# Optimization experiments

Hardware: AMD Instinct MI355X
Metric: run time of the kernel (lower is better)

Reference implementation:

```python
import jax, jax.numpy as jnp
import numpy as np

CUTOFF = 5.0

def cubic_cutoff(d):
    # f(0)=1, f(y)=0, smooth first derivatives at both ends
    y = CUTOFF
    xc = 1.0 - 1.5 * (d * d) / (y * y) + 0.5 * (d * d * d) / (y * y * y)
    return jnp.where(d <= 0.0, 1.0, jnp.where(d >= y, 0.0, xc))


def setup_inputs() -> dict:
    key = jax.random.key(0)
    ks = jax.random.split(key, 16)
    B, N, H = 64, 64, 128
    h = jax.random.normal(ks[0], (B, N, H), jnp.float32)
    x = jax.random.uniform(ks[1], (B, N, 3), jnp.float32) * 10.0  # 10A box -> partial neighbor sparsity
    node_mask = jnp.ones((B, N), dtype=bool)
    h0 = jax.random.normal(ks[2], (B, N, H), jnp.float32)
    s = lambda fin: 1.0 / np.sqrt(fin)
    # edge_mlp: Linear(2H+1 -> H), SiLU, Linear(H -> H), SiLU
    We1 = jax.random.normal(ks[3], (2 * H + 1, H), jnp.float32) * s(2 * H + 1)
    be1 = jnp.zeros((H,), jnp.float32)
    We2 = jax.random.normal(ks[4], (H, H), jnp.float32) * s(H)
    be2 = jnp.zeros((H,), jnp.float32)
    # node_mlp: Linear(H + residual_nf + H = 3H -> H), SiLU, Linear(H -> H)
    Wn1 = jax.random.normal(ks[5], (3 * H, H), jnp.float32) * s(3 * H)
    bn1 = jnp.zeros((H,), jnp.float32)
    Wn2 = jax.random.normal(ks[6], (H, H), jnp.float32) * s(H)
    bn2 = jnp.zeros((H,), jnp.float32)
    # coord_mlp: Linear(H -> H), SiLU, Linear(H -> 1, no bias, xavier gain=0.001)
    Wc1 = jax.random.normal(ks[7], (H, H), jnp.float32) * s(H)
    bc1 = jnp.zeros((H,), jnp.float32)
    Wc2 = jax.random.normal(ks[8], (H, 1), jnp.float32) * (0.001 * s(H))
    return {"h": h, "x": x, "node_mask": node_mask, "h0": h0,
            "We1": We1, "be1": be1, "We2": We2, "be2": be2,
            "Wn1": Wn1, "bn1": bn1, "Wn2": Wn2, "bn2": bn2,
            "Wc1": Wc1, "bc1": bc1, "Wc2": Wc2}


def reference(h, x, node_mask, h0, We1, be1, We2, be2, Wn1, bn1, Wn2, bn2, Wc1, bc1, Wc2):
    B, N, H = h.shape
    # pairwise distances; distances are detached in the torch default path
    diff = x[:, :, None, :] - x[:, None, :, :]                     # [B,N,N,3]
    d = jax.lax.stop_gradient(jnp.sqrt(jnp.sum(diff * diff, -1)))  # [B,N,N]
    eye = jnp.eye(N, dtype=bool)[None]
    mask = (node_mask[:, :, None] & node_mask[:, None, :]
            & (d < CUTOFF) & (~eye))                               # [B,N,N]
    maskf = mask.astype(h.dtype)
    # edge model: feat[b,j,k] = [h[b,j], h[b,k], d^2]
    feat = jnp.concatenate([
        jnp.broadcast_to(h[:, :, None, :], (B, N, N, H)),
        jnp.broadcast_to(h[:, None, :, :], (B, N, N, H)),
        (d * d)[..., None]], axis=-1)                              # [B,N,N,2H+1]
    e = jax.nn.silu(feat @ We1 + be1)
    e = jax.nn.silu(e @ We2 + be2)
    mij = e * (cubic_cutoff(d) * maskf)[..., None]                 # [B,N,N,H]
    # node model: sum messages into receiver j
    mi = jnp.sum(mij, axis=2)                                      # [B,N,H]
    nfeat = jnp.concatenate([h, mi, h0], axis=-1)                  # [B,N,3H]
    h_out = jax.nn.silu(nfeat @ Wn1 + bn1) @ Wn2 + bn2
    h_new = h + h_out                                              # recurrent
    # coord model (scatter-add semantics of the intended math)
    phi = jax.nn.silu(mij @ Wc1 + bc1) @ Wc2                       # [B,N,N,1]
    C = 1.0 / (N - 1.0)
    x_up = C * jnp.sum(diff * phi * maskf[..., None], axis=2)      # [B,N,3]
    x_new = jnp.clip(x + x_up, -1000.0, 1000.0)
    return (h_new, x_new)
```

## Files before the change

kernel.cpp:

```cpp
#include <hip/hip_runtime.h>

#define Hh 128
#define Nn 64

typedef _Float16 f16x8 __attribute__((ext_vector_type(8)));
typedef float f32x4 __attribute__((ext_vector_type(4)));

__device__ __forceinline__ float silu_f(float v){
    return v * __builtin_amdgcn_rcpf(1.0f + __expf(-v));
}
__device__ __forceinline__ int swz(int row, int cb){ return row*256 + (cb ^ ((row & 7) << 4)); }

#define WT_BYTES (9*32768)

__global__ __launch_bounds__(128) void k_w(
    const float* __restrict__ We1, const float* __restrict__ We2, const float* __restrict__ Wc1,
    const float* __restrict__ Wn1, const float* __restrict__ Wn2, char* __restrict__ wT)
{
    if (blockIdx.x == 128){
        if (threadIdx.x < 16){
            f16x8 v;
            #pragma unroll
            for (int i=0;i<8;i++) v[i] = (_Float16)We1[256*Hh + threadIdx.x*8 + i];
            *(f16x8*)(wT + 8*32768 + threadIdx.x*16) = v;
        }
        return;
    }
    const int id  = blockIdx.x*128 + threadIdx.x;
    const int mat = id >> 11;
    const int r   = id & 2047;
    const int n   = r >> 4;
    const int kg  = r & 15;
    const float* __restrict__ src;
    int koff = 0;
    switch (mat){
        case 0: src = We2; break;
        case 1: src = Wc1; break;
        case 2: src = Wn1; break;
        case 3: src = Wn1; koff = 128; break;
        case 4: src = Wn1; koff = 256; break;
        case 5: src = Wn2; break;
        case 6: src = We1; break;
        default: src = We1; koff = 128; break;
    }
    f16x8 v;
    #pragma unroll
    for (int i=0;i<8;i++) v[i] = (_Float16)src[(koff + kg*8 + i)*Hh + n];
    *(f16x8*)(wT + mat*32768 + n*256 + kg*16) = v;
}

__global__ __launch_bounds__(256, 2) void k_preG(
    const float* __restrict__ h, const char* __restrict__ wT, const float* __restrict__ be1,
    _Float16* __restrict__ Aout, _Float16* __restrict__ Bout)
{
    __shared__ __align__(16) char sA[4096];

    const int r0  = blockIdx.x * 16;
    const int tid = threadIdx.x;
    const int w   = tid >> 6;
    const int l   = tid & 63;
    const int lrow= l & 15;
    const int lk  = l >> 4;
    const int n0 = 2*w, n1 = n0 + 1;
    const int colA = n0*16 + lrow, colB = n1*16 + lrow;

    {
        const int row = tid >> 4;
        const int g   = tid & 15;
        const float4* src = (const float4*)(h + (r0+row)*Hh + g*8);
        const float4 v0 = src[0], v1 = src[1];
        f16x8 e;
        e[0]=(_Float16)v0.x; e[1]=(_Float16)v0.y; e[2]=(_Float16)v0.z; e[3]=(_Float16)v0.w;
        e[4]=(_Float16)v1.x; e[5]=(_Float16)v1.y; e[6]=(_Float16)v1.z; e[7]=(_Float16)v1.w;
        *(f16x8*)(sA + swz(row, g*16)) = e;
    }
    __syncthreads();

    const char* WaT = wT + 6*32768;
    const char* WbT = wT + 7*32768;

    f32x4 accA[2], accB[2];
    {
        const float ba = be1[colA], bb = be1[colB];
        accA[0] = (f32x4){ba,ba,ba,ba};
        accA[1] = (f32x4){bb,bb,bb,bb};
        accB[0] = (f32x4){0.f,0.f,0.f,0.f};
        accB[1] = (f32x4){0.f,0.f,0.f,0.f};
    }
    #pragma unroll
    for (int kb=0;kb<4;kb++){
        const int cb = kb*64 + lk*16;
        const f16x8 a   = *(const f16x8*)(sA  + swz(lrow, cb));
        const f16x8 bA0 = *(const f16x8*)(WaT + (n0*16+lrow)*256 + cb);
        const f16x8 bA1 = *(const f16x8*)(WaT + (n1*16+lrow)*256 + cb);
        const f16x8 bB0 = *(const f16x8*)(WbT + (n0*16+lrow)*256 + cb);
        const f16x8 bB1 = *(const f16x8*)(WbT + (n1*16+lrow)*256 + cb);
        accA[0] = __builtin_amdgcn_mfma_f32_16x16x32_f16(a, bA0, accA[0], 0, 0, 0);
        accA[1] = __builtin_amdgcn_mfma_f32_16x16x32_f16(a, bA1, accA[1], 0, 0, 0);
        accB[0] = __builtin_amdgcn_mfma_f32_16x16x32_f16(a, bB0, accB[0], 0, 0, 0);
        accB[1] = __builtin_amdgcn_mfma_f32_16x16x32_f16(a, bB1, accB[1], 0, 0, 0);
    }
    #pragma unroll
    for (int r=0;r<4;r++){
        const int row = r0 + lk*4 + r;
        Aout[row*Hh + colA] = (_Float16)accA[0][r];
        Aout[row*Hh + colB] = (_Float16)accA[1][r];
        Bout[row*Hh + colA] = (_Float16)accB[0][r];
        Bout[row*Hh + colB] = (_Float16)accB[1][r];
    }
}

__global__ __launch_bounds__(256, 2) void k_main(
    const float* __restrict__ x,
    const _Float16* __restrict__ Ain, const _Float16* __restrict__ Bin,
    const char* __restrict__ wT,
    const float* __restrict__ be2_g,
    const float* __restrict__ bc1_g, const float* __restrict__ Wc2,
    _Float16* __restrict__ mi_g,
    float* __restrict__ out_x)
{
    __shared__ __align__(16) char sEM[32768];
    __shared__ float sCut[2][Nn], sD2[2][Nn];
    __shared__ float sDx0[2][Nn], sDx1[2][Nn], sDx2[2][Nn];
    __shared__ int   sList[2][Nn];
    __shared__ int   sNvA[2];
    __shared__ float sPhP[4][128];

    const int bj0 = blockIdx.x * 2;
    const int b   = bj0 >> 6;
    const int j0  = bj0 & 63;
    const int tid = threadIdx.x;
    const int w   = tid >> 6;
    const int l   = tid & 63;
    const int lrow= l & 15;
    const int lk  = l >> 4;

    if (tid < 128){
        const int seg = tid >> 6;
        const int idx = tid & 63;
        const int jj  = j0 + seg;
        const int bjj = bj0 + seg;
        const float xj0v = x[bjj*3+0], xj1v = x[bjj*3+1], xj2v = x[bjj*3+2];
        const float dx0 = xj0v - x[(b*Nn+idx)*3+0];
        const float dx1 = xj1v - x[(b*Nn+idx)*3+1];
        const float dx2 = xj2v - x[(b*Nn+idx)*3+2];
        const float d2 = dx0*dx0 + dx1*dx1 + dx2*dx2;
        const bool valid = (idx != jj) && (d2 < 25.0f);
        const unsigned long long bal = __ballot(valid);
        const int pos = __popcll(bal & ((1ull << idx) - 1ull));
        if (valid){
            sList[seg][pos] = idx;
            sD2[seg][pos]   = d2;
            sDx0[seg][pos]  = dx0; sDx1[seg][pos] = dx1; sDx2[seg][pos] = dx2;
            const float d = sqrtf(d2);
            sCut[seg][pos]  = 1.0f - 0.06f*d2 + 0.004f*d2*d;
        }
        if (idx == 0) sNvA[seg] = (int)__popcll(bal);
    }
    __syncthreads();
    const int nv1 = __builtin_amdgcn_readfirstlane(sNvA[0]);
    const int nv2 = __builtin_amdgcn_readfirstlane(sNvA[1]);
    const int nvt = nv1 + nv2;
    const int MT  = (nvt + 15) >> 4;
    const int R16 = MT << 4;

    {
        const f16x8* W6 = (const f16x8*)(wT + 8*32768);
        #pragma unroll
        for (int pass=0; pass<2; pass++){
            const int row = pass*64 + (tid >> 2);
            if (row < R16){
                const int q = tid & 3;
                const bool vrow = row < nvt;
                const int seg = (row < nv1) ? 0 : 1;
                const int idx = (row < nv1) ? row : row - nv1;
                const int k   = vrow ? sList[seg][idx] : 0;
                const _Float16 d2h = vrow ? (_Float16)sD2[seg][idx] : (_Float16)0.0f;
                f16x8 dsplat;
                #pragma unroll
                for (int i=0;i<8;i++) dsplat[i] = d2h;
                const f16x8* Aj = (const f16x8*)(Ain + (bj0+seg)*Hh + q*32);
                const f16x8* Bk = (const f16x8*)(Bin + (b*Nn+k)*Hh + q*32);
                #pragma unroll
                for (int s=0;s<4;s++){
                    f16x8 pre = Aj[s] + Bk[s] + W6[q*4+s]*dsplat;
                    f16x8 e;
                    #pragma unroll
                    for (int i=0;i<8;i++){
                        const float v = (float)pre[i];
                        e[i] = (_Float16)silu_f(v);
                    }
                    *(f16x8*)(sEM + swz(row, q*64 + s*16)) = e;
                }
            }
        }
    }
    __syncthreads();

    const int n0 = 2*w, n1 = n0 + 1;
    const int colA = n0*16 + lrow, colB = n1*16 + lrow;
    const char* We2T = wT;
    const char* Wc1T = wT + 32768;

    float mia0 = 0.f, mib0 = 0.f, mia1 = 0.f, mib1 = 0.f;
    f32x4 acc[4][2];

    for (int tb = 0; tb < MT; tb += 4){
        const int MTp = (MT - tb < 4) ? (MT - tb) : 4;
        {
            const float b2a = be2_g[colA], b2b = be2_g[colB];
            #pragma unroll
            for (int mt=0;mt<4;mt++){
                acc[mt][0] = (f32x4){b2a,b2a,b2a,b2a};
                acc[mt][1] = (f32x4){b2b,b2b,b2b,b2b};
            }
        }
        #pragma unroll
        for (int kb=0;kb<4;kb++){
            const int cb = kb*64 + lk*16;
            const f16x8 bA = *(const f16x8*)(We2T + (n0*16+lrow)*256 + cb);
            const f16x8 bB = *(const f16x8*)(We2T + (n1*16+lrow)*256 + cb);
            #pragma unroll
            for (int mt=0;mt<4;mt++){
                if (mt < MTp){
                    const f16x8 a = *(const f16x8*)(sEM + swz((tb+mt)*16 + lrow, cb));
                    acc[mt][0] = __builtin_amdgcn_mfma_f32_16x16x32_f16(a, bA, acc[mt][0], 0, 0, 0);
                    acc[mt][1] = __builtin_amdgcn_mfma_f32_16x16x32_f16(a, bB, acc[mt][1], 0, 0, 0);
                }
            }
        }
        #pragma unroll
        for (int mt=0;mt<4;mt++){
            if (mt < MTp){
                const int tlo = (tb+mt)*16;
                const bool pure0 = (tlo + 16 <= nv1);
                const bool pure1 = (tlo >= nv1);
                #pragma unroll
                for (int r=0;r<4;r++){
                    const int row = tlo + lk*4 + r;
                    const bool vrow = row < nvt;
                    const int seg = (row < nv1) ? 0 : 1;
                    const int idx = (row < nv1) ? row : row - nv1;
                    const float cut = vrow ? sCut[seg][idx] : 0.f;
                    const float m0 = silu_f(acc[mt][0][r]) * cut;
                    const float m1 = silu_f(acc[mt][1][r]) * cut;
                    acc[mt][0][r] = m0; acc[mt][1][r] = m1;
                    if (pure0){ mia0 += m0; mib0 += m1; }
                    else if (pure1){ mia1 += m0; mib1 += m1; }
                    else {
                        mia0 += (row < nv1) ? m0 : 0.f;
                        mib0 += (row < nv1) ? m1 : 0.f;
                        mia1 += (row < nv1) ? 0.f : m0;
                        mib1 += (row < nv1) ? 0.f : m1;
                    }
                }
            }
        }
        __syncthreads();
        #pragma unroll
        for (int mt=0;mt<4;mt++){
            if (mt < MTp){
                #pragma unroll
                for (int r=0;r<4;r++){
                    const int row = (tb+mt)*16 + lk*4 + r;
                    const int xr  = (row & 7) << 4;
                    *(_Float16*)(sEM + row*256 + ((colA*2) ^ xr)) = (_Float16)acc[mt][0][r];
                    *(_Float16*)(sEM + row*256 + ((colB*2) ^ xr)) = (_Float16)acc[mt][1][r];
                }
            }
        }
    }
    {
        mia0 += __shfl_xor(mia0, 16); mia0 += __shfl_xor(mia0, 32);
        mib0 += __shfl_xor(mib0, 16); mib0 += __shfl_xor(mib0, 32);
        mia1 += __shfl_xor(mia1, 16); mia1 += __shfl_xor(mia1, 32);
        mib1 += __shfl_xor(mib1, 16); mib1 += __shfl_xor(mib1, 32);
        if (l < 16){
            mi_g[bj0*Hh + colA]     = (_Float16)mia0;
            mi_g[bj0*Hh + colB]     = (_Float16)mib0;
            mi_g[(bj0+1)*Hh + colA] = (_Float16)mia1;
            mi_g[(bj0+1)*Hh + colB] = (_Float16)mib1;
        }
    }
    __syncthreads();

    for (int tb = 0; tb < MT; tb += 4){
        const int MTp = (MT - tb < 4) ? (MT - tb) : 4;
        {
            const float c1a = bc1_g[colA], c1b = bc1_g[colB];
            #pragma unroll
            for (int mt=0;mt<4;mt++){
                acc[mt][0] = (f32x4){c1a,c1a,c1a,c1a};
                acc[mt][1] = (f32x4){c1b,c1b,c1b,c1b};
            }
        }
        #pragma unroll
        for (int kb=0;kb<4;kb++){
            const int cb = kb*64 + lk*16;
            const f16x8 bA = *(const f16x8*)(Wc1T + (n0*16+lrow)*256 + cb);
            const f16x8 bB = *(const f16x8*)(Wc1T + (n1*16+lrow)*256 + cb);
            #pragma unroll
            for (int mt=0;mt<4;mt++){
                if (mt < MTp){
                    const f16x8 a = *(const f16x8*)(sEM + swz((tb+mt)*16 + lrow, cb));
                    acc[mt][0] = __builtin_amdgcn_mfma_f32_16x16x32_f16(a, bA, acc[mt][0], 0, 0, 0);
                    acc[mt][1] = __builtin_amdgcn_mfma_f32_16x16x32_f16(a, bB, acc[mt][1], 0, 0, 0);
                }
            }
        }
        const float wca = Wc2[colA], wcb = Wc2[colB];
        float php[16];
        #pragma unroll
        for (int mt=0;mt<4;mt++){
            if (mt < MTp){
                #pragma unroll
                for (int r=0;r<4;r++)
                    php[mt*4+r] = silu_f(acc[mt][0][r])*wca + silu_f(acc[mt][1][r])*wcb;
            }
        }
        #pragma unroll
        for (int i=0;i<16;i++){
            if ((i>>2) < MTp){
                php[i] += __shfl_xor(php[i], 1);
                php[i] += __shfl_xor(php[i], 2);
                php[i] += __shfl_xor(php[i], 4);
                php[i] += __shfl_xor(php[i], 8);
            }
        }
        if (lrow == 0){
            #pragma unroll
            for (int mt=0;mt<4;mt++){
                if (mt < MTp){
                    #pragma unroll
                    for (int r=0;r<4;r++)
                        sPhP[w][(tb+mt)*16 + lk*4 + r] = php[mt*4+r];
                }
            }
        }
    }
    __syncthreads();

    if (tid < 128){
        const int seg = tid >> 6;
        const int t   = tid & 63;
        const int nvg = seg ? nv2 : nv1;
        float v0=0.f, v1=0.f, v2=0.f;
        if (t < nvg){
            const int row = seg ? (nv1 + t) : t;
            const float phi = sPhP[0][row] + sPhP[1][row] + sPhP[2][row] + sPhP[3][row];
            v0 = sDx0[seg][t] * phi;
            v1 = sDx1[seg][t] * phi;
            v2 = sDx2[seg][t] * phi;
        }
        #pragma unroll
        for (int off=1; off<64; off<<=1){
            v0 += __shfl_xor(v0, off);
            v1 += __shfl_xor(v1, off);
            v2 += __shfl_xor(v2, off);
        }
        if (t == 0){
            const int bjj = bj0 + seg;
            const float C = 1.0f/63.0f;
            out_x[bjj*3+0] = fminf(fmaxf(x[bjj*3+0] + C*v0, -1000.f), 1000.f);
            out_x[bjj*3+1] = fminf(fmaxf(x[bjj*3+1] + C*v1, -1000.f), 1000.f);
            out_x[bjj*3+2] = fminf(fmaxf(x[bjj*3+2] + C*v2, -1000.f), 1000.f);
        }
    }
}

__global__ __launch_bounds__(256, 2) void k_node(
    const float* __restrict__ h, const _Float16* __restrict__ mi_g,
    const float* __restrict__ h0,
    const char* __restrict__ wT,
    const float* __restrict__ bn1_g, const float* __restrict__ bn2_g,
    float* __restrict__ out_h)
{
    __shared__ __align__(16) char sA[8192];
    __shared__ __align__(16) char sHid[8192];

    const int r0  = blockIdx.x * 32;
    const int tid = threadIdx.x;
    const int w   = tid >> 6;
    const int l   = tid & 63;
    const int lrow= l & 15;
    const int lk  = l >> 4;
    const int n0 = 2*w, n1 = n0 + 1;
    const int colA = n0*16 + lrow, colB = n1*16 + lrow;

    f32x4 acc[2][2];
    {
        const float b1a = bn1_g[colA], b1b = bn1_g[colB];
        acc[0][0] = (f32x4){b1a,b1a,b1a,b1a};
        acc[0][1] = (f32x4){b1b,b1b,b1b,b1b};
        acc[1][0] = (f32x4){b1a,b1a,b1a,b1a};
        acc[1][1] = (f32x4){b1b,b1b,b1b,b1b};
    }

    const int arow = tid >> 3;
    const int g    = tid & 7;

    for (int c = 0; c < 3; c++){
        if (c == 1){
            const f16x8* src = (const f16x8*)(mi_g + (r0+arow)*Hh + g*16);
            *(f16x8*)(sA + swz(arow, g*32))      = src[0];
            *(f16x8*)(sA + swz(arow, g*32+16))   = src[1];
        } else {
            const float* base = (c == 0) ? h : h0;
            const float4* src = (const float4*)(base + (r0+arow)*Hh + g*16);
            const float4 v0=src[0], v1=src[1], v2=src[2], v3=src[3];
            f16x8 e0, e1;
            e0[0]=(_Float16)v0.x; e0[1]=(_Float16)v0.y; e0[2]=(_Float16)v0.z; e0[3]=(_Float16)v0.w;
            e0[4]=(_Float16)v1.x; e0[5]=(_Float16)v1.y; e0[6]=(_Float16)v1.z; e0[7]=(_Float16)v1.w;
            e1[0]=(_Float16)v2.x; e1[1]=(_Float16)v2.y; e1[2]=(_Float16)v2.z; e1[3]=(_Float16)v2.w;
            e1[4]=(_Float16)v3.x; e1[5]=(_Float16)v3.y; e1[6]=(_Float16)v3.z; e1[7]=(_Float16)v3.w;
            *(f16x8*)(sA + swz(arow, g*32))    = e0;
            *(f16x8*)(sA + swz(arow, g*32+16)) = e1;
        }
        __syncthreads();
        const char* Wimg = wT + (2+c)*32768;
        #pragma unroll
        for (int kb=0;kb<4;kb++){
            const int cb = kb*64 + lk*16;
            const f16x8 bA = *(const f16x8*)(Wimg + (n0*16+lrow)*256 + cb);
            const f16x8 bB = *(const f16x8*)(Wimg + (n1*16+lrow)*256 + cb);
            #pragma unroll
            for (int mt=0;mt<2;mt++){
                const f16x8 a = *(const f16x8*)(sA + swz(mt*16 + lrow, cb));
                acc[mt][0] = __builtin_amdgcn_mfma_f32_16x16x32_f16(a, bA, acc[mt][0], 0, 0, 0);
                acc[mt][1] = __builtin_amdgcn_mfma_f32_16x16x32_f16(a, bB, acc[mt][1], 0, 0, 0);
            }
        }
        __syncthreads();
    }

    #pragma unroll
    for (int mt=0;mt<2;mt++){
        #pragma unroll
        for (int r=0;r<4;r++){
            const int row = mt*16 + lk*4 + r;
            const int xr  = (row & 7) << 4;
            *(_Float16*)(sHid + row*256 + ((colA*2) ^ xr)) = (_Float16)silu_f(acc[mt][0][r]);
            *(_Float16*)(sHid + row*256 + ((colB*2) ^ xr)) = (_Float16)silu_f(acc[mt][1][r]);
        }
    }
    __syncthreads();

    const char* Wn2T = wT + 5*32768;
    f32x4 acc2[2][2];
    {
        const float b2a = bn2_g[colA], b2b = bn2_g[colB];
        acc2[0][0] = (f32x4){b2a,b2a,b2a,b2a};
        acc2[0][1] = (f32x4){b2b,b2b,b2b,b2b};
        acc2[1][0] = (f32x4){b2a,b2a,b2a,b2a};
        acc2[1][1] = (f32x4){b2b,b2b,b2b,b2b};
    }
    #pragma unroll
    for (int kb=0;kb<4;kb++){
        const int cb = kb*64 + lk*16;
        const f16x8 bA = *(const f16x8*)(Wn2T + (n0*16+lrow)*256 + cb);
        const f16x8 bB = *(const f16x8*)(Wn2T + (n1*16+lrow)*256 + cb);
        #pragma unroll
        for (int mt=0;mt<2;mt++){
            const f16x8 a = *(const f16x8*)(sHid + swz(mt*16 + lrow, cb));
            acc2[mt][0] = __builtin_amdgcn_mfma_f32_16x16x32_f16(a, bA, acc2[mt][0], 0, 0, 0);
            acc2[mt][1] = __builtin_amdgcn_mfma_f32_16x16x32_f16(a, bB, acc2[mt][1], 0, 0, 0);
        }
    }
    #pragma unroll
    for (int mt=0;mt<2;mt++){
        #pragma unroll
        for (int r=0;r<4;r++){
            const int row = r0 + mt*16 + lk*4 + r;
            out_h[row*Hh + colA] = h[row*Hh + colA] + acc2[mt][0][r];
            out_h[row*Hh + colB] = h[row*Hh + colB] + acc2[mt][1][r];
        }
    }
}

extern "C" void kernel_launch(void* const* d_in, const int* in_sizes, int n_in,
                              void* d_out, int out_size, void* d_ws, size_t ws_size,
                              hipStream_t stream) {
    const float* h   = (const float*)d_in[0];
    const float* x   = (const float*)d_in[1];
    const float* h0  = (const float*)d_in[3];
    const float* We1 = (const float*)d_in[4];
    const float* be1 = (const float*)d_in[5];
    const float* We2 = (const float*)d_in[6];
    const float* be2 = (const float*)d_in[7];
    const float* Wn1 = (const float*)d_in[8];
    const float* bn1 = (const float*)d_in[9];
    const float* Wn2 = (const float*)d_in[10];
    const float* bn2 = (const float*)d_in[11];
    const float* Wc1 = (const float*)d_in[12];
    const float* bc1 = (const float*)d_in[13];
    const float* Wc2 = (const float*)d_in[14];

    float* out_h = (float*)d_out;
    float* out_x = out_h + 64*64*128;

    char*      wT = (char*)d_ws;
    _Float16*  A  = (_Float16*)(wT + WT_BYTES);
    _Float16*  Bv = A + 4096*128;
    _Float16*  mi = Bv + 4096*128;

    k_w   <<<129, 128, 0, stream>>>(We1, We2, Wc1, Wn1, Wn2, wT);
    k_preG<<<256, 256, 0, stream>>>(h, wT, be1, A, Bv);
    k_main<<<2048, 256, 0, stream>>>(x, A, Bv, wT, be2, bc1, Wc2, mi, out_x);
    k_node<<<128, 256, 0, stream>>>(h, mi, h0, wT, bn1, bn2, out_h);
}
```

Before: 91.29 us.

## Pack per-batch compacted edge lists into 128-row tiles for edge MLP

```diff
diff --git a/kernel.cpp b/kernel.cpp
--- a/kernel.cpp
+++ b/kernel.cpp
@@ -2,9 +2,12 @@
 
 #define Hh 128
 #define Nn 64
+#define CAP 2048
+#define TPB 16
 
 typedef _Float16 f16x8 __attribute__((ext_vector_type(8)));
 typedef float f32x4 __attribute__((ext_vector_type(4)));
+typedef unsigned int u32;
 
 __device__ __forceinline__ float silu_f(float v){
     return v * __builtin_amdgcn_rcpf(1.0f + __expf(-v));
@@ -110,86 +113,139 @@
     }
 }
 
-__global__ __launch_bounds__(256, 2) void k_main(
+__global__ __launch_bounds__(256) void k_prep(
     const float* __restrict__ x,
+    u32* __restrict__ cntB, u32* __restrict__ off_g, u32* __restrict__ cnt_g,
+    u32* __restrict__ code_g, float* __restrict__ d2_g, float* __restrict__ cut_g)
+{
+    __shared__ float sX[192];
+    __shared__ int sCnt[64], sOff[64];
+    const int b   = blockIdx.x;
+    const int tid = threadIdx.x;
+    const int wd  = tid >> 6;
+    const int l   = tid & 63;
+
+    if (tid < 192) sX[tid] = x[b*192 + tid];
+    __syncthreads();
+
+    for (int jj = 0; jj < 16; jj++){
+        const int j = wd*16 + jj;
+        const float dx0 = sX[j*3+0]-sX[l*3+0];
+        const float dx1 = sX[j*3+1]-sX[l*3+1];
+        const float dx2 = sX[j*3+2]-sX[l*3+2];
+        const float d2 = dx0*dx0 + dx1*dx1 + dx2*dx2;
+        const bool valid = (l != j) && (d2 < 25.0f);
+        const unsigned long long bal = __ballot(valid);
+        if (l == 0) sCnt[j] = (int)__popcll(bal);
+    }
+    __syncthreads();
+    if (tid < 64){
+        int v = sCnt[tid];
+        int incl = v;
+        #pragma unroll
+        for (int off=1; off<64; off<<=1){
+            int o = __shfl_up(incl, off);
+            if (l >= off) incl += o;
+        }
+        sOff[tid] = incl - v;
+    }
+    __syncthreads();
+    if (tid < 64){
+        off_g[b*64 + tid] = (u32)sOff[tid];
+        cnt_g[b*64 + tid] = (u32)sCnt[tid];
+        if (tid == 63){
+            int tot = sOff[63] + sCnt[63];
+            cntB[b] = (u32)(tot > CAP ? CAP : tot);
+        }
+    }
+    for (int jj = 0; jj < 16; jj++){
+        const int j = wd*16 + jj;
+        const float dx0 = sX[j*3+0]-sX[l*3+0];
+        const float dx1 = sX[j*3+1]-sX[l*3+1];
+        const float dx2 = sX[j*3+2]-sX[l*3+2];
+        const float d2 = dx0*dx0 + dx1*dx1 + dx2*dx2;
+        const bool valid = (l != j) && (d2 < 25.0f);
+        const unsigned long long bal = __ballot(valid);
+        const int pos = __popcll(bal & ((1ull << l) - 1ull));
+        if (valid){
+            const int dst = sOff[j] + pos;
+            if (dst < CAP){
+                const int e = b*CAP + dst;
+                code_g[e] = (u32)((j << 6) | l);
+                d2_g[e]   = d2;
+                cut_g[e]  = 1.0f - 0.06f*d2 + 0.004f*d2*sqrtf(d2);
+            }
+        }
+    }
+}
+
+__global__ __launch_bounds__(256, 2) void k_edge(
     const _Float16* __restrict__ Ain, const _Float16* __restrict__ Bin,
     const char* __restrict__ wT,
-    const float* __restrict__ be2_g,
-    const float* __restrict__ bc1_g, const float* __restrict__ Wc2,
-    _Float16* __restrict__ mi_g,
-    float* __restrict__ out_x)
+    const float* __restrict__ be2_g, const float* __restrict__ bc1_g, const float* __restrict__ Wc2,
+    const u32* __restrict__ cntB, const u32* __restrict__ code_g,
+    const float* __restrict__ d2_g, const float* __restrict__ cut_g,
+    float* __restrict__ mi_p, float* __restrict__ phi_g)
 {
     __shared__ __align__(16) char sEM[32768];
-    __shared__ float sCut[2][Nn], sD2[2][Nn];
-    __shared__ float sDx0[2][Nn], sDx1[2][Nn], sDx2[2][Nn];
-    __shared__ int   sList[2][Nn];
-    __shared__ int   sNvA[2];
+    __shared__ int   sBj[128];
+    __shared__ u32   sCode[128];
+    __shared__ float sD2[128], sCut[128];
     __shared__ float sPhP[4][128];
 
-    const int bj0 = blockIdx.x * 2;
-    const int b   = bj0 >> 6;
-    const int j0  = bj0 & 63;
+    const int bid = blockIdx.x;
+    const int b   = bid & 63;
+    const int t   = bid >> 6;
+    const int E_b = (int)cntB[b];
+    const int r0  = t*128;
+    if (r0 >= E_b) return;
+    const int R   = (E_b - r0 < 128) ? (E_b - r0) : 128;
+    const int MT  = (R + 15) >> 4;
+
     const int tid = threadIdx.x;
     const int w   = tid >> 6;
     const int l   = tid & 63;
     const int lrow= l & 15;
     const int lk  = l >> 4;
+    const int n0 = 2*w, n1 = n0 + 1;
+    const int colA = n0*16 + lrow, colB = n1*16 + lrow;
+    const char* We2T = wT;
+    const char* Wc1T = wT + 32768;
 
     if (tid < 128){
-        const int seg = tid >> 6;
-        const int idx = tid & 63;
-        const int jj  = j0 + seg;
-        const int bjj = bj0 + seg;
-        const float xj0v = x[bjj*3+0], xj1v = x[bjj*3+1], xj2v = x[bjj*3+2];
-        const float dx0 = xj0v - x[(b*Nn+idx)*3+0];
-        const float dx1 = xj1v - x[(b*Nn+idx)*3+1];
-        const float dx2 = xj2v - x[(b*Nn+idx)*3+2];
-        const float d2 = dx0*dx0 + dx1*dx1 + dx2*dx2;
-        const bool valid = (idx != jj) && (d2 < 25.0f);
-        const unsigned long long bal = __ballot(valid);
-        const int pos = __popcll(bal & ((1ull << idx) - 1ull));
-        if (valid){
-            sList[seg][pos] = idx;
-            sD2[seg][pos]   = d2;
-            sDx0[seg][pos]  = dx0; sDx1[seg][pos] = dx1; sDx2[seg][pos] = dx2;
-            const float d = sqrtf(d2);
-            sCut[seg][pos]  = 1.0f - 0.06f*d2 + 0.004f*d2*d;
-        }
-        if (idx == 0) sNvA[seg] = (int)__popcll(bal);
-    }
-    __syncthreads();
-    const int nv1 = __builtin_amdgcn_readfirstlane(sNvA[0]);
-    const int nv2 = __builtin_amdgcn_readfirstlane(sNvA[1]);
-    const int nvt = nv1 + nv2;
-    const int MT  = (nvt + 15) >> 4;
-    const int R16 = MT << 4;
+        if (tid < R){
+            const u32 c = code_g[b*CAP + r0 + tid];
+            sCode[tid] = c;
+            sBj[tid]   = (int)(c >> 6);
+            sD2[tid]   = d2_g[b*CAP + r0 + tid];
+            sCut[tid]  = cut_g[b*CAP + r0 + tid];
+        } else {
+            sCode[tid] = 0; sBj[tid] = -1; sD2[tid] = 0.f; sCut[tid] = 0.f;
+        }
+    }
+    __syncthreads();
 
     {
         const f16x8* W6 = (const f16x8*)(wT + 8*32768);
         #pragma unroll
         for (int pass=0; pass<2; pass++){
             const int row = pass*64 + (tid >> 2);
-            if (row < R16){
+            if (row < MT*16){
                 const int q = tid & 3;
-                const bool vrow = row < nvt;
-                const int seg = (row < nv1) ? 0 : 1;
-                const int idx = (row < nv1) ? row : row - nv1;
-                const int k   = vrow ? sList[seg][idx] : 0;
-                const _Float16 d2h = vrow ? (_Float16)sD2[seg][idx] : (_Float16)0.0f;
+                const u32 c = sCode[row];
+                const int jl = (int)(c >> 6), kl = (int)(c & 63);
+                const _Float16 d2h = (_Float16)sD2[row];
                 f16x8 dsplat;
                 #pragma unroll
                 for (int i=0;i<8;i++) dsplat[i] = d2h;
-                const f16x8* Aj = (const f16x8*)(Ain + (bj0+seg)*Hh + q*32);
-                const f16x8* Bk = (const f16x8*)(Bin + (b*Nn+k)*Hh + q*32);
+                const f16x8* Aj = (const f16x8*)(Ain + (b*Nn+jl)*Hh + q*32);
+                const f16x8* Bk = (const f16x8*)(Bin + (b*Nn+kl)*Hh + q*32);
                 #pragma unroll
                 for (int s=0;s<4;s++){
                     f16x8 pre = Aj[s] + Bk[s] + W6[q*4+s]*dsplat;
                     f16x8 e;
                     #pragma unroll
-                    for (int i=0;i<8;i++){
-                        const float v = (float)pre[i];
-                        e[i] = (_Float16)silu_f(v);
-                    }
+                    for (int i=0;i<8;i++) e[i] = (_Float16)silu_f((float)pre[i]);
                     *(f16x8*)(sEM + swz(row, q*64 + s*16)) = e;
                 }
             }
@@ -197,14 +253,7 @@
     }
     __syncthreads();
 
-    const int n0 = 2*w, n1 = n0 + 1;
-    const int colA = n0*16 + lrow, colB = n1*16 + lrow;
-    const char* We2T = wT;
-    const char* Wc1T = wT + 32768;
-
-    float mia0 = 0.f, mib0 = 0.f, mia1 = 0.f, mib1 = 0.f;
     f32x4 acc[4][2];
-
     for (int tb = 0; tb < MT; tb += 4){
         const int MTp = (MT - tb < 4) ? (MT - tb) : 4;
         {
@@ -232,27 +281,12 @@
         #pragma unroll
         for (int mt=0;mt<4;mt++){
             if (mt < MTp){
-                const int tlo = (tb+mt)*16;
-                const bool pure0 = (tlo + 16 <= nv1);
-                const bool pure1 = (tlo >= nv1);
                 #pragma unroll
                 for (int r=0;r<4;r++){
-                    const int row = tlo + lk*4 + r;
-                    const bool vrow = row < nvt;
-                    const int seg = (row < nv1) ? 0 : 1;
-                    const int idx = (row < nv1) ? row : row - nv1;
-                    const float cut = vrow ? sCut[seg][idx] : 0.f;
-                    const float m0 = silu_f(acc[mt][0][r]) * cut;
-                    const float m1 = silu_f(acc[mt][1][r]) * cut;
+                    const int row = (tb+mt)*16 + lk*4 + r;
+                    const float m0 = silu_f(acc[mt][0][r]) * sCut[row];
+                    const float m1 = silu_f(acc[mt][1][r]) * sCut[row];
                     acc[mt][0][r] = m0; acc[mt][1][r] = m1;
-                    if (pure0){ mia0 += m0; mib0 += m1; }
-                    else if (pure1){ mia1 += m0; mib1 += m1; }
-                    else {
-                        mia0 += (row < nv1) ? m0 : 0.f;
-                        mib0 += (row < nv1) ? m1 : 0.f;
-                        mia1 += (row < nv1) ? 0.f : m0;
-                        mib1 += (row < nv1) ? 0.f : m1;
-                    }
                 }
             }
         }
@@ -270,19 +304,26 @@
             }
         }
     }
+    __syncthreads();
+
     {
-        mia0 += __shfl_xor(mia0, 16); mia0 += __shfl_xor(mia0, 32);
-        mib0 += __shfl_xor(mib0, 16); mib0 += __shfl_xor(mib0, 32);
-        mia1 += __shfl_xor(mia1, 16); mia1 += __shfl_xor(mia1, 32);
-        mib1 += __shfl_xor(mib1, 16); mib1 += __shfl_xor(mib1, 32);
-        if (l < 16){
-            mi_g[bj0*Hh + colA]     = (_Float16)mia0;
-            mi_g[bj0*Hh + colB]     = (_Float16)mib0;
-            mi_g[(bj0+1)*Hh + colA] = (_Float16)mia1;
-            mi_g[(bj0+1)*Hh + colB] = (_Float16)mib1;
-        }
-    }
-    __syncthreads();
+        const int col  = tid & 127;
+        const int half = tid >> 7;
+        const int slot = (t & 1)*2 + half;
+        float sum = 0.f;
+        int cur = -1;
+        const int rbeg = half*64, rend = rbeg + 64;
+        for (int r = rbeg; r < rend; ++r){
+            const int bj = sBj[r];
+            const float m = (float)(*(const _Float16*)(sEM + r*256 + ((col*2) ^ ((r&7)<<4))));
+            if (bj != cur){
+                if (cur >= 0) mi_p[((size_t)slot*4096 + (b<<6) + cur)*128 + col] = sum;
+                cur = bj; sum = 0.f;
+            }
+            sum += m;
+        }
+        if (cur >= 0) mi_p[((size_t)slot*4096 + (b<<6) + cur)*128 + col] = sum;
+    }
 
     for (int tb = 0; tb < MT; tb += 4){
         const int MTp = (MT - tb < 4) ? (MT - tb) : 4;
@@ -340,31 +381,56 @@
     }
     __syncthreads();
 
-    if (tid < 128){
-        const int seg = tid >> 6;
-        const int t   = tid & 63;
-        const int nvg = seg ? nv2 : nv1;
-        float v0=0.f, v1=0.f, v2=0.f;
-        if (t < nvg){
-            const int row = seg ? (nv1 + t) : t;
-            const float phi = sPhP[0][row] + sPhP[1][row] + sPhP[2][row] + sPhP[3][row];
-            v0 = sDx0[seg][t] * phi;
-            v1 = sDx1[seg][t] * phi;
-            v2 = sDx2[seg][t] * phi;
-        }
-        #pragma unroll
-        for (int off=1; off<64; off<<=1){
-            v0 += __shfl_xor(v0, off);
-            v1 += __shfl_xor(v1, off);
-            v2 += __shfl_xor(v2, off);
-        }
-        if (t == 0){
-            const int bjj = bj0 + seg;
-            const float C = 1.0f/63.0f;
-            out_x[bjj*3+0] = fminf(fmaxf(x[bjj*3+0] + C*v0, -1000.f), 1000.f);
-            out_x[bjj*3+1] = fminf(fmaxf(x[bjj*3+1] + C*v1, -1000.f), 1000.f);
-            out_x[bjj*3+2] = fminf(fmaxf(x[bjj*3+2] + C*v2, -1000.f), 1000.f);
-        }
+    if (tid < 128 && tid < R){
+        const float phi = sPhP[0][tid] + sPhP[1][tid] + sPhP[2][tid] + sPhP[3][tid];
+        phi_g[b*CAP + r0 + tid] = phi;
+    }
+}
+
+__global__ __launch_bounds__(256) void k_reduce(
+    const float* __restrict__ x,
+    const u32* __restrict__ off_g, const u32* __restrict__ cnt_g,
+    const u32* __restrict__ code_g, const float* __restrict__ phi_g,
+    const float* __restrict__ mi_p,
+    _Float16* __restrict__ mi_g, float* __restrict__ out_x)
+{
+    const int tid = threadIdx.x;
+    const int wd  = tid >> 6;
+    const int l   = tid & 63;
+    const int gid = blockIdx.x*4 + wd;
+    const int b   = gid >> 6;
+
+    #pragma unroll
+    for (int p=0;p<2;p++){
+        const int col = l*2 + p;
+        const size_t base = (size_t)gid*128 + col;
+        const float s = mi_p[base] + mi_p[(size_t)4096*128 + base]
+                      + mi_p[(size_t)2*4096*128 + base] + mi_p[(size_t)3*4096*128 + base];
+        mi_g[gid*Hh + col] = (_Float16)s;
+    }
+
+    const int cnt = (int)cnt_g[gid];
+    const int off = (int)off_g[gid];
+    float v0=0.f, v1=0.f, v2=0.f;
+    if (l < cnt && (off + l) < CAP){
+        const int e = b*CAP + off + l;
+        const int kl = (int)(code_g[e] & 63);
+        const float phi = phi_g[e];
+        v0 = (x[gid*3+0] - x[(b*Nn+kl)*3+0]) * phi;
+        v1 = (x[gid*3+1] - x[(b*Nn+kl)*3+1]) * phi;
+        v2 = (x[gid*3+2] - x[(b*Nn+kl)*3+2]) * phi;
+    }
+    #pragma unroll
+    for (int off2=1; off2<64; off2<<=1){
+        v0 += __shfl_xor(v0, off2);
+        v1 += __shfl_xor(v1, off2);
+        v2 += __shfl_xor(v2, off2);
+    }
+    if (l == 0){
+        const float C = 1.0f/63.0f;
+        out_x[gid*3+0] = fminf(fmaxf(x[gid*3+0] + C*v0, -1000.f), 1000.f);
+        out_x[gid*3+1] = fminf(fmaxf(x[gid*3+1] + C*v1, -1000.f), 1000.f);
+        out_x[gid*3+2] = fminf(fmaxf(x[gid*3+2] + C*v2, -1000.f), 1000.f);
     }
 }
 
@@ -498,13 +564,25 @@
     float* out_h = (float*)d_out;
     float* out_x = out_h + 64*64*128;
 
-    char*      wT = (char*)d_ws;
-    _Float16*  A  = (_Float16*)(wT + WT_BYTES);
-    _Float16*  Bv = A + 4096*128;
-    _Float16*  mi = Bv + 4096*128;
-
-    k_w   <<<129, 128, 0, stream>>>(We1, We2, Wc1, Wn1, Wn2, wT);
-    k_preG<<<256, 256, 0, stream>>>(h, wT, be1, A, Bv);
-    k_main<<<2048, 256, 0, stream>>>(x, A, Bv, wT, be2, bc1, Wc2, mi, out_x);
-    k_node<<<128, 256, 0, stream>>>(h, mi, h0, wT, bn1, bn2, out_h);
-}
+    char*      wT   = (char*)d_ws;
+    _Float16*  A    = (_Float16*)(wT + WT_BYTES);
+    _Float16*  Bv   = A + 4096*128;
+    _Float16*  mi   = Bv + 4096*128;
+    u32*       cntB = (u32*)(mi + 4096*128);
+    u32*       offg = cntB + 64;
+    u32*       cntg = offg + 4096;
+    u32*       code = cntg + 4096;
+    float*     d2g  = (float*)(code + 64*CAP);
+    float*     cutg = d2g + 64*CAP;
+    float*     phig = cutg + 64*CAP;
+    float*     mip  = phig + 64*CAP;
+
+    hipMemsetAsync(mip, 0, (size_t)4*4096*128*sizeof(float), stream);
+    k_w     <<<129, 128, 0, stream>>>(We1, We2, Wc1, Wn1, Wn2, wT);
+    k_preG  <<<256, 256, 0, stream>>>(h, wT, be1, A, Bv);
+    k_prep  <<<64, 256, 0, stream>>>(x, cntB, offg, cntg, code, d2g, cutg);
+    k_edge  <<<64*TPB, 256, 0, stream>>>(A, Bv, wT, be2, bc1, Wc2,
+                                         cntB, code, d2g, cutg, mip, phig);
+    k_reduce<<<1024, 256, 0, stream>>>(x, offg, cntg, code, phig, mip, mi, out_x);
+    k_node  <<<128, 256, 0, stream>>>(h, mi, h0, wT, bn1, bn2, out_h);
+}
```

After: 93.04 us. No clear change (+1.9%).
